# Kernel optimization log

Measured on AMD Instinct MI355X. Metric: run time of the kernel, lower is better.

Reference implementation:

```python
import jax, jax.numpy as jnp
import numpy as np

N_VERTICES = 50000
N_RADIAL = 5
N_ANGULAR = 8
FEATURE_DIM = 64
AMT_TEMPLATES = 64
TEMPLATE_RADIUS = 0.03
ROTATION_DELTA = 1


def create_template_matrix(n_radial, n_angular, radius):
    # Polar grid of template vertices in cartesian coordinates: (R, A, 2)
    radii = radius * (np.arange(1, n_radial + 1) / n_radial)
    angles = 2.0 * np.pi * np.arange(n_angular) / n_angular
    x = radii[:, None] * np.cos(angles)[None, :]
    y = radii[:, None] * np.sin(angles)[None, :]
    return np.stack([x, y], axis=-1).astype(np.float32)


def define_interpolation_coefficients(template_matrix):
    # Gaussian interpolation prior (concrete instance of the abstract method),
    # normalized over all template vertices. Shape: (R, A, R, A)
    R, A, _ = template_matrix.shape
    flat = template_matrix.reshape(R * A, 2)
    d2 = ((flat[:, None, :] - flat[None, :, :]) ** 2).sum(-1)  # (RA, RA)
    sigma = TEMPLATE_RADIUS / N_RADIAL
    w = np.exp(-d2 / (2.0 * sigma ** 2))
    w = w / w.sum(axis=1, keepdims=True)
    return w.reshape(R, A, R, A).astype(np.float32)


def setup_inputs() -> dict:
    key = jax.random.key(0)
    k1, k2, k3, k4, k5, k6, k7 = jax.random.split(key, 7)
    mesh_signal = jax.random.normal(k1, (N_VERTICES, FEATURE_DIM), dtype=jnp.float32)
    # barycentric coordinates: [..., 0] = vertex index (stored as float),
    # [..., 1] = barycentric weight summing to 1 over the 3 triangle corners
    idx = jax.random.randint(k2, (N_VERTICES, N_RADIAL, N_ANGULAR, 3), 0, N_VERTICES)
    w = jax.random.uniform(k3, (N_VERTICES, N_RADIAL, N_ANGULAR, 3), dtype=jnp.float32)
    w = w / jnp.sum(w, axis=-1, keepdims=True)
    bary_coordinates = jnp.stack([idx.astype(jnp.float32), w], axis=-1)
    neighbor_weights = jax.random.normal(
        k4, (AMT_TEMPLATES, N_RADIAL, N_ANGULAR, FEATURE_DIM), dtype=jnp.float32) * 0.05
    center_weights = jax.random.normal(
        k5, (AMT_TEMPLATES, 1, FEATURE_DIM), dtype=jnp.float32) * 0.05
    bias = jax.random.normal(k6, (AMT_TEMPLATES,), dtype=jnp.float32) * 0.05
    tmpl = create_template_matrix(N_RADIAL, N_ANGULAR, TEMPLATE_RADIUS)
    interp_coeff = jnp.asarray(
        define_interpolation_coefficients(tmpl).reshape(N_RADIAL, N_ANGULAR, N_RADIAL * N_ANGULAR))
    return {
        "mesh_signal": mesh_signal,
        "bary_coordinates": bary_coordinates,
        "neighbor_weights": neighbor_weights,
        "center_weights": center_weights,
        "bias": bias,
        "interp_coeff": interp_coeff,
    }


def reference(mesh_signal, bary_coordinates, neighbor_weights, center_weights, bias, interp_coeff):
    N, R, A, _, _ = bary_coordinates.shape
    C = mesh_signal.shape[-1]
    T = neighbor_weights.shape[0]

    # ---- patch operator: barycentric gather + interpolation ----
    idx = bary_coordinates[..., 0].astype(jnp.int32)          # (N, R, A, 3)
    bw = bary_coordinates[..., 1]                              # (N, R, A, 3)
    gathered = mesh_signal[idx]                                # (N, R, A, 3, C)
    interp = jnp.sum(bw[..., None] * gathered, axis=-2)        # (N, R, A, C)

    # ---- prior: matvec with interpolation coefficients ----
    # original: (N,1,1,C,RA) matvec (R,A,RA) -> (N,R,A,C)
    ms = interp.reshape(N, R * A, C)                           # (N, RA, C)
    interp = jnp.einsum('nmc,ram->nrac', ms, interp_coeff)     # (N, R, A, C)

    # ---- center fold: einsum('si,tji->sjt') ----
    conv_center = jnp.einsum('nc,tjc->njt', mesh_signal, center_weights)  # (N, 1, T)

    # ---- neighbor fold over rotations ----
    # roll(interp, shift=r, axis=angular) . W == interp . roll(W, shift=-r, axis=angular)
    rotations = np.arange(0, A, ROTATION_DELTA)
    w_rot = jnp.stack([jnp.roll(neighbor_weights, -int(r), axis=2) for r in rotations])  # (O, T, R, A, C)
    conv_neighbor = jnp.einsum('nrac,otrac->not', interp, w_rot) + bias                  # (N, O, T)

    return jax.nn.relu(conv_center + conv_neighbor)
```

## Files before the change

kernel.cpp:

```cpp
#include <hip/hip_runtime.h>
#include <hip/hip_bf16.h>

#define N_V   50000
#define KTOT  2624
#define NOUT  512
#define NKB   41
#define BM    128
#define BN    256

typedef short v8s __attribute__((ext_vector_type(8)));
typedef float v4f __attribute__((ext_vector_type(4)));
typedef unsigned int v4u __attribute__((ext_vector_type(4)));
typedef unsigned short u16;
typedef unsigned int u32;

__device__ __forceinline__ u16 f2bf(float f) {
    u32 u = __float_as_uint(f);
    return (u16)((u + 0x7FFFu + ((u >> 16) & 1u)) >> 16);
}

__device__ __forceinline__ void gl2lds(const u16* g, u16* l) {
    __builtin_amdgcn_global_load_lds(
        (const __attribute__((address_space(1))) u32*)(uintptr_t)g,
        (__attribute__((address_space(3))) u32*)(uintptr_t)l, 16, 0, 0);
}

__device__ __forceinline__ u32 ipair(u32 pa, u32 pb, u32 pc, float w0, float w1, float w2) {
    float a0 = __uint_as_float(pa << 16), a1 = __uint_as_float(pa & 0xffff0000u);
    float b0 = __uint_as_float(pb << 16), b1 = __uint_as_float(pb & 0xffff0000u);
    float c0 = __uint_as_float(pc << 16), c1 = __uint_as_float(pc & 0xffff0000u);
    float r0 = w0 * a0 + w1 * b0 + w2 * c0;
    float r1 = w0 * a1 + w1 * b1 + w2 * c1;
    return __builtin_amdgcn_perm(__float_as_uint(r1) + 0x8000u,
                                 __float_as_uint(r0) + 0x8000u, 0x07060302u);
}

__global__ void cast_ms(const float* __restrict__ ms, u16* __restrict__ msb,
                        u16* __restrict__ Xc) {
    int i = (blockIdx.x * 256 + threadIdx.x) * 4;
    float4 v = *reinterpret_cast<const float4*>(ms + i);
    ushort4 o;
    o.x = f2bf(v.x); o.y = f2bf(v.y); o.z = f2bf(v.z); o.w = f2bf(v.w);
    *reinterpret_cast<ushort4*>(msb + i) = o;
    if (Xc) {
        int n = i >> 6, c = i & 63;
        *reinterpret_cast<ushort4*>(Xc + (size_t)n * KTOT + 2560 + c) = o;
    }
}

__global__ void build_w2(const float* __restrict__ nw, const float* __restrict__ cw,
                         const float* __restrict__ coeff, u16* __restrict__ w2) {
    int l = blockIdx.x * 256 + threadIdx.x;
    if (l >= NOUT * KTOT) return;
    int j = l / KTOT, k = l - j * KTOT;
    int o = j >> 6, t = j & 63;
    u16 v;
    if (k >= 2560) {
        v = f2bf(cw[t * 64 + (k - 2560)]);
    } else {
        int m = k >> 6, c = k & 63;
        float s = 0.f;
        #pragma unroll
        for (int ra = 0; ra < 40; ++ra) {
            int r = ra >> 3, a = ra & 7;
            s += coeff[ra * 40 + m] * nw[((t * 5 + r) * 8 + ((a + o) & 7)) * 64 + c];
        }
        v = f2bf(s);
    }
    w2[l] = v;
}

__global__ void build_x(const float* __restrict__ bary, const u16* __restrict__ msb,
                        u16* __restrict__ X) {
    u32 t = blockIdx.x * 256 + threadIdx.x;
    u32 n = t / 160u;
    u32 rem = t - n * 160u;
    u32 m = rem >> 2, j = rem & 3;
    const float* bb = bary + (size_t)n * 240 + m * 6;
    float2 p0 = *(const float2*)(bb);
    float2 p1 = *(const float2*)(bb + 2);
    float2 p2 = *(const float2*)(bb + 4);
    u32 jb = j * 32u;
    u32 o0 = ((u32)(int)p0.x) * 128u + jb;
    u32 o1 = ((u32)(int)p1.x) * 128u + jb;
    u32 o2 = ((u32)(int)p2.x) * 128u + jb;
    const char* mb = (const char*)msb;
    v4u a0 = *(const v4u*)(mb + o0), b0 = *(const v4u*)(mb + o0 + 16);
    v4u a1 = *(const v4u*)(mb + o1), b1 = *(const v4u*)(mb + o1 + 16);
    v4u a2 = *(const v4u*)(mb + o2), b2 = *(const v4u*)(mb + o2 + 16);
    v4u c0, c1;
    #pragma unroll
    for (int e = 0; e < 4; ++e) {
        c0[e] = ipair(a0[e], a1[e], a2[e], p0.y, p1.y, p2.y);
        c1[e] = ipair(b0[e], b1[e], b2[e], p0.y, p1.y, p2.y);
    }
    char* xp = (char*)X + (size_t)n * (KTOT * 2) + m * 128 + jb;
    *(v4u*)xp = c0;
    *(v4u*)(xp + 16) = c1;
}

__global__ __launch_bounds__(512, 4)
void gemm2(const u16* __restrict__ X, const u16* __restrict__ w2,
           const float* __restrict__ bias, float* __restrict__ out) {
    __shared__ u16 At[BM * 64];
    __shared__ u16 Bt[BN * 64];

    const int tid  = threadIdx.x;
    const int lane = tid & 63, wave = tid >> 6;
    const int l15  = lane & 15, q = lane >> 4;
    const int wm   = wave >> 2, wn = wave & 3;

    const int id = blockIdx.x;
    const int p  = (id & 7) + 8 * (id >> 4);
    const int by = (id >> 3) & 1;
    if (p >= 391) return;
    const int row0 = p * BM, col0 = by * BN;

    u32 aoff[2];
    #pragma unroll
    for (int h = 0; h < 2; ++h) {
        int slot = wave * 128 + h * 64 + lane;
        int arow = slot >> 3, ablk = (slot & 7) ^ (arow & 7);
        int grow = row0 + arow; if (grow > N_V - 1) grow = N_V - 1;
        aoff[h] = (u32)grow * (u32)KTOT + (u32)(ablk * 8);
    }
    u32 boff[4];
    #pragma unroll
    for (int i = 0; i < 4; ++i) {
        int slot = wave * 256 + i * 64 + lane;
        int brow = slot >> 3, bblk = (slot & 7) ^ (brow & 7);
        boff[i] = (u32)(col0 + brow) * (u32)KTOT + (u32)(bblk * 8);
    }

    const int eq = l15 & 7;
    const u32 a_rd0 = (u32)(wm * 64 + l15) * 128 + (u32)((q ^ eq) * 16);
    const u32 b_rd0 = (u32)(wn * 64 + l15) * 128 + (u32)((q ^ eq) * 16);

    v4f acc[4][4];
    #pragma unroll
    for (int mi = 0; mi < 4; ++mi)
        #pragma unroll
        for (int ni = 0; ni < 4; ++ni)
            acc[mi][ni] = (v4f){0.f, 0.f, 0.f, 0.f};

    #pragma unroll 1
    for (int kb = 0; kb < NKB; ++kb) {
        __syncthreads();
        #pragma unroll
        for (int h = 0; h < 2; ++h)
            gl2lds(X + aoff[h] + kb * 64, &At[wave * 1024 + h * 512]);
        #pragma unroll
        for (int i = 0; i < 4; ++i)
            gl2lds(w2 + boff[i] + kb * 64, &Bt[wave * 2048 + i * 512]);
        __syncthreads();

        const char* atp = (const char*)At;
        const char* btp = (const char*)Bt;
        #pragma unroll
        for (int s = 0; s < 2; ++s) {
            u32 ao = a_rd0 ^ (u32)(s * 64), bo = b_rd0 ^ (u32)(s * 64);
            v8s a_f[4], b_f[4];
            #pragma unroll
            for (int mi = 0; mi < 4; ++mi) a_f[mi] = *(const v8s*)(atp + ao + mi * 2048);
            #pragma unroll
            for (int ni = 0; ni < 4; ++ni) b_f[ni] = *(const v8s*)(btp + bo + ni * 2048);
            #pragma unroll
            for (int mi = 0; mi < 4; ++mi)
                #pragma unroll
                for (int ni = 0; ni < 4; ++ni)
                    acc[mi][ni] = __builtin_amdgcn_mfma_f32_16x16x32_bf16(
                        a_f[mi], b_f[ni], acc[mi][ni], 0, 0, 0);
        }
    }

    float bv[4];
    #pragma unroll
    for (int ni = 0; ni < 4; ++ni) bv[ni] = bias[ni * 16 + l15];
    #pragma unroll
    for (int mi = 0; mi < 4; ++mi) {
        int rbase = row0 + wm * 64 + mi * 16 + q * 4;
        #pragma unroll
        for (int ni = 0; ni < 4; ++ni) {
            int cg = col0 + wn * 64 + ni * 16 + l15;
            #pragma unroll
            for (int rg = 0; rg < 4; ++rg) {
                int rr = rbase + rg;
                if (rr < N_V) {
                    float v = acc[mi][ni][rg] + bv[ni];
                    out[(size_t)rr * NOUT + cg] = v > 0.f ? v : 0.f;
                }
            }
        }
    }
}

__global__ __launch_bounds__(512, 2)
void gemm_fused(const float* __restrict__ bary, const u16* __restrict__ msb,
                const u16* __restrict__ w2, const float* __restrict__ bias,
                float* __restrict__ out) {
    __shared__ u16 At[BM * 64];
    __shared__ u16 Bt[2 * BN * 64];

    const int tid  = threadIdx.x;
    const int lane = tid & 63, wave = tid >> 6;
    const int l15  = lane & 15, q = lane >> 4;
    const int wm   = wave >> 2, wn = wave & 3;

    const int id  = blockIdx.x;
    const int bx  = id % 391, by = id / 391;
    const int row0 = bx * BM, col0 = by * BN;

    const int ar  = tid >> 2;
    const u32 acb = (u32)(tid & 3) * 32;
    int an = row0 + ar; if (an > N_V - 1) an = N_V - 1;
    const u32* brow = (const u32*)bary + (size_t)an * 240;
    const u32 an_off = (u32)an * 128 + acb;

    const int e_a = ar & 7;
    const u32 at_w0 = (u32)ar * 128 + (u32)(((2 * (tid & 3)) ^ e_a) * 16);
    const u32 at_w1 = at_w0 ^ 16;

    const int eq = l15 & 7;
    const u32 a_rd0 = (u32)(wm * 64 + l15) * 128 + (u32)((q ^ eq) * 16);
    const u32 b_rd0 = (u32)(wn * 64 + l15) * 128 + (u32)((q ^ eq) * 16);

    const int rl = lane >> 3;
    const int bl = (lane & 7) ^ rl;

    v4f acc[4][4];
    #pragma unroll
    for (int mi = 0; mi < 4; ++mi)
        #pragma unroll
        for (int ni = 0; ni < 4; ++ni)
            acc[mi][ni] = (v4f){0.f, 0.f, 0.f, 0.f};

    v4u G0_0a, G0_0b, G0_1a, G0_1b, G0_2a, G0_2b;
    v4u G1_0a, G1_0b, G1_1a, G1_1b, G1_2a, G1_2b;
    v4u B0lo, B0hi, B1lo, B1hi;
    float w00, w01, w02, w10, w11, w12;
    v4u cv0, cv1;

#define BARY_LOAD(DLO, DHI, kc) do { \
    u32 _d0 = ((u32)((kc) * 6)) & ~3u; \
    DLO = *(const v4u*)(brow + _d0); \
    DHI = *(const v4u*)(brow + _d0 + 4); } while (0)

#define DECODE_ISSUE(PAR, BLO, BHI, Ga0, Gb0, Ga1, Gb1, Ga2, Gb2, W0, W1, W2) do { \
    u32 uf0, uw0, uf1, uw1, uf2, uw2; \
    if (PAR) { uf0 = BLO[2]; uw0 = BLO[3]; uf1 = BHI[0]; uw1 = BHI[1]; uf2 = BHI[2]; uw2 = BHI[3]; } \
    else     { uf0 = BLO[0]; uw0 = BLO[1]; uf1 = BLO[2]; uw1 = BLO[3]; uf2 = BHI[0]; uw2 = BHI[1]; } \
    u32 _o0 = ((u32)(int)__uint_as_float(uf0) << 7) + acb; \
    u32 _o1 = ((u32)(int)__uint_as_float(uf1) << 7) + acb; \
    u32 _o2 = ((u32)(int)__uint_as_float(uf2) << 7) + acb; \
    const char* _mb = (const char*)msb; \
    Ga0 = *(const v4u*)(_mb + _o0); Gb0 = *(const v4u*)(_mb + _o0 + 16); \
    Ga1 = *(const v4u*)(_mb + _o1); Gb1 = *(const v4u*)(_mb + _o1 + 16); \
    Ga2 = *(const v4u*)(_mb + _o2); Gb2 = *(const v4u*)(_mb + _o2 + 16); \
    W0 = __uint_as_float(uw0); W1 = __uint_as_float(uw1); W2 = __uint_as_float(uw2); } while (0)

#define CONVERT(Ga0, Gb0, Ga1, Gb1, Ga2, Gb2, W0, W1, W2) do { \
    _Pragma("unroll") \
    for (int _j = 0; _j < 4; ++_j) { \
        cv0[_j] = ipair(Ga0[_j], Ga1[_j], Ga2[_j], W0, W1, W2); \
        cv1[_j] = ipair(Gb0[_j], Gb1[_j], Gb2[_j], W0, W1, W2); } } while (0)

#define BLDS(KB_LD, BUF) do { \
    _Pragma("unroll") \
    for (int _ii = 0; _ii < 4; ++_ii) { \
        int _we = wave * 4 + _ii; \
        u32 _src = (u32)(col0 + _we * 8 + rl) * KTOT + (u32)(KB_LD) * 64 + (u32)(bl * 8); \
        gl2lds(w2 + _src, &Bt[(BUF) * (BN * 64) + _we * 512]); } } while (0)

#define AT_STORE() do { \
    *(v4u*)((char*)At + at_w0) = cv0; \
    *(v4u*)((char*)At + at_w1) = cv1; } while (0)

#define MFMA_STEP(BUF) do { \
    const char* _atp = (const char*)At; \
    const char* _btp = (const char*)Bt + (BUF) * (BN * 64 * 2); \
    _Pragma("unroll") \
    for (int _s = 0; _s < 2; ++_s) { \
        u32 _ao = a_rd0 ^ (u32)(_s * 64), _bo = b_rd0 ^ (u32)(_s * 64); \
        v8s _af[4], _bf[4]; \
        _Pragma("unroll") \
        for (int _mi = 0; _mi < 4; ++_mi) _af[_mi] = *(const v8s*)(_atp + _ao + _mi * 2048); \
        _Pragma("unroll") \
        for (int _ni = 0; _ni < 4; ++_ni) _bf[_ni] = *(const v8s*)(_btp + _bo + _ni * 2048); \
        _Pragma("unroll") \
        for (int _mi = 0; _mi < 4; ++_mi) \
            _Pragma("unroll") \
            for (int _ni = 0; _ni < 4; ++_ni) \
                acc[_mi][_ni] = __builtin_amdgcn_mfma_f32_16x16x32_bf16( \
                    _af[_mi], _bf[_ni], acc[_mi][_ni], 0, 0, 0); } } while (0)

#define BAR2_12() asm volatile("s_waitcnt vmcnt(12) lgkmcnt(0)\ns_barrier" ::: "memory")
#define BAR2_10() asm volatile("s_waitcnt vmcnt(10) lgkmcnt(0)\ns_barrier" ::: "memory")
#define BAR2_6()  asm volatile("s_waitcnt vmcnt(6) lgkmcnt(0)\ns_barrier"  ::: "memory")
#define BAR2_4()  asm volatile("s_waitcnt vmcnt(4) lgkmcnt(0)\ns_barrier"  ::: "memory")
#define BAR2_0()  asm volatile("s_waitcnt vmcnt(0) lgkmcnt(0)\ns_barrier"  ::: "memory")
#define BAR1()    asm volatile("s_barrier" ::: "memory")

    BARY_LOAD(B0lo, B0hi, 0);
    DECODE_ISSUE(0, B0lo, B0hi, G0_0a, G0_0b, G0_1a, G0_1b, G0_2a, G0_2b, w00, w01, w02);
    BARY_LOAD(B1lo, B1hi, 1);
    DECODE_ISSUE(1, B1lo, B1hi, G1_0a, G1_0b, G1_1a, G1_1b, G1_2a, G1_2b, w10, w11, w12);
    BARY_LOAD(B0lo, B0hi, 2);
    BLDS(0, 0);

    #pragma unroll 1
    for (int i = 0; i < 20; ++i) {
        {
            const int kb = 2 * i;
            CONVERT(G0_0a, G0_0b, G0_1a, G0_1b, G0_2a, G0_2b, w00, w01, w02);
            if (kb <= 36) BARY_LOAD(B1lo, B1hi, kb + 3);
            if (kb <= 37) {
                DECODE_ISSUE(0, B0lo, B0hi, G0_0a, G0_0b, G0_1a, G0_1b, G0_2a, G0_2b,
                             w00, w01, w02);
            } else if (kb == 38) {
                G0_0a = *(const v4u*)((const char*)msb + an_off);
                G0_0b = *(const v4u*)((const char*)msb + an_off + 16);
            }
            BAR1();
            BLDS(kb + 1, 1);
            AT_STORE();
            if (kb <= 36) BAR2_12(); else BAR2_6();
            MFMA_STEP(0);
        }
        {
            const int kb = 2 * i + 1;
            CONVERT(G1_0a, G1_0b, G1_1a, G1_1b, G1_2a, G1_2b, w10, w11, w12);
            if (kb <= 36) BARY_LOAD(B0lo, B0hi, kb + 3);
            if (kb <= 37)
                DECODE_ISSUE(1, B1lo, B1hi, G1_0a, G1_0b, G1_1a, G1_1b, G1_2a, G1_2b,
                             w10, w11, w12);
            BAR1();
            BLDS(kb + 1, 0);
            AT_STORE();
            if (kb <= 36) BAR2_12();
            else if (kb == 37) BAR2_10();
            else BAR2_4();
            MFMA_STEP(1);
        }
    }
    {
        cv0 = G0_0a; cv1 = G0_0b;
        BAR1();
        AT_STORE();
        BAR2_0();
        MFMA_STEP(0);
    }

    float bv[4];
    #pragma unroll
    for (int ni = 0; ni < 4; ++ni) bv[ni] = bias[ni * 16 + l15];
    #pragma unroll
    for (int mi = 0; mi < 4; ++mi) {
        int rbase = row0 + wm * 64 + mi * 16 + q * 4;
        #pragma unroll
        for (int ni = 0; ni < 4; ++ni) {
            int cg = col0 + wn * 64 + ni * 16 + l15;
            #pragma unroll
            for (int rg = 0; rg < 4; ++rg) {
                int rr = rbase + rg;
                if (rr < N_V) {
                    float v = acc[mi][ni][rg] + bv[ni];
                    out[(size_t)rr * NOUT + cg] = v > 0.f ? v : 0.f;
                }
            }
        }
    }
}

extern "C" void kernel_launch(void* const* d_in, const int* in_sizes, int n_in,
                              void* d_out, int out_size, void* d_ws, size_t ws_size,
                              hipStream_t stream) {
    const float* ms    = (const float*)d_in[0];
    const float* bary  = (const float*)d_in[1];
    const float* nw    = (const float*)d_in[2];
    const float* cw    = (const float*)d_in[3];
    const float* bias  = (const float*)d_in[4];
    const float* coeff = (const float*)d_in[5];
    float* out = (float*)d_out;

    u16* msb = (u16*)d_ws;
    u16* w2  = (u16*)((char*)d_ws + 6400000);
    const size_t x_off  = 9087104;
    const size_t x_need = x_off + (size_t)N_V * KTOT * 2;
    u16* X = (u16*)((char*)d_ws + x_off);

    if (ws_size >= x_need) {
        cast_ms<<<3125, 256, 0, stream>>>(ms, msb, X);
        build_w2<<<(NOUT * KTOT + 255) / 256, 256, 0, stream>>>(nw, cw, coeff, w2);
        build_x<<<31250, 256, 0, stream>>>(bary, msb, X);
        gemm2<<<784, 512, 0, stream>>>(X, w2, bias, out);
    } else {
        cast_ms<<<3125, 256, 0, stream>>>(ms, msb, (u16*)nullptr);
        build_w2<<<(NOUT * KTOT + 255) / 256, 256, 0, stream>>>(nw, cw, coeff, w2);
        gemm_fused<<<782, 512, 0, stream>>>(bary, msb, w2, bias, out);
    }
}
```

Before: 452.7 us.

## Add 256x256-tile GEMM with 4-stage LDS pipeline using dynamic shared memory

Adds a new GEMM kernel that uses 256x256 output tiles with a K-step of 32 and a four-buffer global-to-LDS prefetch ring in 128KB of dynamic shared memory. Compute overlaps with loads three stages ahead, gated by vmcnt waits, and MFMA issue runs under raised wave priority. The larger tile doubles operand reuse per block and halves the grid, at the cost of lower occupancy (two blocks per CU by launch bound, fewer waves in practice because of LDS use) and more accumulator registers. The old GEMM is kept as a fallback if the dynamic LDS attribute cannot be set.

```diff
diff --git a/kernel.cpp b/kernel.cpp
--- a/kernel.cpp
+++ b/kernel.cpp
@@ -7,6 +7,7 @@
 #define NKB   41
 #define BM    128
 #define BN    256
+#define KT32  82
 
 typedef short v8s __attribute__((ext_vector_type(8)));
 typedef float v4f __attribute__((ext_vector_type(4)));
@@ -99,6 +100,108 @@
     *(v4u*)(xp + 16) = c1;
 }
 
+#define WBAR(N) asm volatile("s_waitcnt vmcnt(" #N ")\n\ts_barrier" ::: "memory")
+
+__global__ __launch_bounds__(512, 2)
+void gemm3(const u16* __restrict__ X, const u16* __restrict__ w2,
+           const float* __restrict__ bias, float* __restrict__ out) {
+    extern __shared__ char lds[];
+
+    const int tid  = threadIdx.x;
+    const int lane = tid & 63, wave = tid >> 6;
+    const int l15  = lane & 15, q = lane >> 4;
+    const int wm   = wave >> 2, wn = wave & 3;
+
+    const int id = blockIdx.x;
+    const int p  = (id & 7) + 8 * (id >> 4);
+    const int by = (id >> 3) & 1;
+    if (p >= 196) return;
+    const int row0 = p * 256, col0 = by * 256;
+
+    u32 aoff[2], boff[2];
+    #pragma unroll
+    for (int h = 0; h < 2; ++h) {
+        int slot = (wave * 2 + h) * 64 + lane;
+        int row  = slot >> 2, b = slot & 3;
+        int g    = b ^ ((row >> 1) & 3);
+        int grow = row0 + row; if (grow > N_V - 1) grow = N_V - 1;
+        aoff[h] = (u32)grow * (u32)KTOT + (u32)(g * 8);
+        boff[h] = (u32)(col0 + row) * (u32)KTOT + (u32)(g * 8);
+    }
+
+    const int sw = (l15 >> 1) & 3;
+    const u32 a_rd0 = (u32)(wm * 128 + l15) * 64u + (u32)((q ^ sw) * 16);
+    const u32 b_rd0 = (u32)(wn * 64  + l15) * 64u + (u32)((q ^ sw) * 16);
+
+    v4f acc[8][4];
+    #pragma unroll
+    for (int mi = 0; mi < 8; ++mi)
+        #pragma unroll
+        for (int ni = 0; ni < 4; ++ni)
+            acc[mi][ni] = (v4f){0.f, 0.f, 0.f, 0.f};
+
+#define STG(T, BUF) do { \
+    const u32 _ko = (u32)(T) * 32u; \
+    _Pragma("unroll") \
+    for (int _h = 0; _h < 2; ++_h) { \
+        gl2lds(X  + aoff[_h] + _ko, (u16*)(lds + (BUF) * 16384 + (wave * 2 + _h) * 1024)); \
+        gl2lds(w2 + boff[_h] + _ko, (u16*)(lds + 65536 + (BUF) * 16384 + (wave * 2 + _h) * 1024)); \
+    } } while (0)
+
+#define CMP(BUF) do { \
+    const char* _ap = lds + (BUF) * 16384; \
+    const char* _bp = lds + 65536 + (BUF) * 16384; \
+    v8s _bf[4], _af[8]; \
+    _Pragma("unroll") \
+    for (int _ni = 0; _ni < 4; ++_ni) _bf[_ni] = *(const v8s*)(_bp + b_rd0 + _ni * 1024); \
+    _Pragma("unroll") \
+    for (int _mi = 0; _mi < 8; ++_mi) _af[_mi] = *(const v8s*)(_ap + a_rd0 + _mi * 1024); \
+    __builtin_amdgcn_s_setprio(1); \
+    _Pragma("unroll") \
+    for (int _mi = 0; _mi < 8; ++_mi) \
+        _Pragma("unroll") \
+        for (int _ni = 0; _ni < 4; ++_ni) \
+            acc[_mi][_ni] = __builtin_amdgcn_mfma_f32_16x16x32_bf16( \
+                _af[_mi], _bf[_ni], acc[_mi][_ni], 0, 0, 0); \
+    __builtin_amdgcn_s_setprio(0); \
+} while (0)
+
+    STG(0, 0); STG(1, 1); STG(2, 2);
+
+    #pragma unroll 1
+    for (int t = 0; t < KT32 - 3; ++t) {
+        WBAR(8);
+        STG(t + 3, (t + 3) & 3);
+        CMP(t & 3);
+    }
+    WBAR(8); CMP(3);
+    WBAR(4); CMP(0);
+    WBAR(0); CMP(1);
+
+#undef STG
+#undef CMP
+
+    float bv[4];
+    #pragma unroll
+    for (int ni = 0; ni < 4; ++ni) bv[ni] = bias[ni * 16 + l15];
+    #pragma unroll
+    for (int mi = 0; mi < 8; ++mi) {
+        int rbase = row0 + wm * 128 + mi * 16 + q * 4;
+        #pragma unroll
+        for (int ni = 0; ni < 4; ++ni) {
+            int cg = col0 + wn * 64 + ni * 16 + l15;
+            #pragma unroll
+            for (int rg = 0; rg < 4; ++rg) {
+                int rr = rbase + rg;
+                if (rr < N_V) {
+                    float v = acc[mi][ni][rg] + bv[ni];
+                    out[(size_t)rr * NOUT + cg] = v > 0.f ? v : 0.f;
+                }
+            }
+        }
+    }
+}
+
 __global__ __launch_bounds__(512, 4)
 void gemm2(const u16* __restrict__ X, const u16* __restrict__ w2,
            const float* __restrict__ bias, float* __restrict__ out) {
@@ -389,10 +492,19 @@
     u16* X = (u16*)((char*)d_ws + x_off);
 
     if (ws_size >= x_need) {
+        static int dyn_ok = -1;
+        if (dyn_ok < 0) {
+            dyn_ok = (hipFuncSetAttribute((const void*)gemm3,
+                          hipFuncAttributeMaxDynamicSharedMemorySize,
+                          131072) == hipSuccess) ? 1 : 0;
+        }
         cast_ms<<<3125, 256, 0, stream>>>(ms, msb, X);
         build_w2<<<(NOUT * KTOT + 255) / 256, 256, 0, stream>>>(nw, cw, coeff, w2);
         build_x<<<31250, 256, 0, stream>>>(bary, msb, X);
-        gemm2<<<784, 512, 0, stream>>>(X, w2, bias, out);
+        if (dyn_ok)
+            gemm3<<<400, 512, 131072, stream>>>(X, w2, bias, out);
+        else
+            gemm2<<<784, 512, 0, stream>>>(X, w2, bias, out);
     } else {
         cast_ms<<<3125, 256, 0, stream>>>(ms, msb, (u16*)nullptr);
         build_w2<<<(NOUT * KTOT + 255) / 256, 256, 0, stream>>>(nw, cw, coeff, w2);
```

Result: slower. 464.9 us (+2.7%).

## Replace GEMM with 256x256-tile double-buffered 4-wave MFMA kernel

Applied to the files above, without the earlier changes.

Replaces the 128x256-tile, 8-wave GEMM with a 256x256 tile computed by 4 waves, each holding a 128x128 accumulator block. K is stepped in chunks of 32, and LDS is double-buffered so the global-to-LDS loads for the next step overlap the MFMAs of the current one. The kernel also uses a different XOR swizzle and raises wave priority around the MFMA bursts. The goal is more data reuse per LDS load and better latency hiding, at the cost of heavy register pressure (likely one block per CU) and a coarse grid of 392 active blocks that may balance poorly across CUs.

```diff
diff --git a/kernel.cpp b/kernel.cpp
--- a/kernel.cpp
+++ b/kernel.cpp
@@ -7,6 +7,7 @@
 #define NKB   41
 #define BM    128
 #define BN    256
+#define KT32  82
 
 typedef short v8s __attribute__((ext_vector_type(8)));
 typedef float v4f __attribute__((ext_vector_type(4)));
@@ -99,89 +100,94 @@
     *(v4u*)(xp + 16) = c1;
 }
 
-__global__ __launch_bounds__(512, 4)
-void gemm2(const u16* __restrict__ X, const u16* __restrict__ w2,
+__global__ __launch_bounds__(256, 2)
+void gemm4(const u16* __restrict__ X, const u16* __restrict__ w2,
            const float* __restrict__ bias, float* __restrict__ out) {
-    __shared__ u16 At[BM * 64];
-    __shared__ u16 Bt[BN * 64];
+    __shared__ u16 sh[32768];
 
     const int tid  = threadIdx.x;
     const int lane = tid & 63, wave = tid >> 6;
     const int l15  = lane & 15, q = lane >> 4;
-    const int wm   = wave >> 2, wn = wave & 3;
+    const int wm   = wave >> 1, wn = wave & 1;
 
     const int id = blockIdx.x;
     const int p  = (id & 7) + 8 * (id >> 4);
     const int by = (id >> 3) & 1;
-    if (p >= 391) return;
-    const int row0 = p * BM, col0 = by * BN;
-
-    u32 aoff[2];
-    #pragma unroll
-    for (int h = 0; h < 2; ++h) {
-        int slot = wave * 128 + h * 64 + lane;
-        int arow = slot >> 3, ablk = (slot & 7) ^ (arow & 7);
-        int grow = row0 + arow; if (grow > N_V - 1) grow = N_V - 1;
-        aoff[h] = (u32)grow * (u32)KTOT + (u32)(ablk * 8);
-    }
-    u32 boff[4];
+    if (p >= 196) return;
+    const int row0 = p * 256, col0 = by * 256;
+
+    u32 aoff[4], boff[4];
     #pragma unroll
     for (int i = 0; i < 4; ++i) {
-        int slot = wave * 256 + i * 64 + lane;
-        int brow = slot >> 3, bblk = (slot & 7) ^ (brow & 7);
-        boff[i] = (u32)(col0 + brow) * (u32)KTOT + (u32)(bblk * 8);
-    }
-
-    const int eq = l15 & 7;
-    const u32 a_rd0 = (u32)(wm * 64 + l15) * 128 + (u32)((q ^ eq) * 16);
-    const u32 b_rd0 = (u32)(wn * 64 + l15) * 128 + (u32)((q ^ eq) * 16);
-
-    v4f acc[4][4];
-    #pragma unroll
-    for (int mi = 0; mi < 4; ++mi)
+        int s   = i * 256 + tid;
+        int row = s >> 2, b = s & 3;
+        int g   = b ^ ((row >> 1) & 3);
+        int grow = row0 + row; if (grow > N_V - 1) grow = N_V - 1;
+        aoff[i] = (u32)grow * (u32)KTOT + (u32)(g * 8);
+        boff[i] = (u32)(col0 + row) * (u32)KTOT + (u32)(g * 8);
+    }
+
+    const int sw = (l15 >> 1) & 3;
+    const u32 a_rd0 = (u32)(wm * 128 + l15) * 64u + (u32)((q ^ sw) * 16);
+    const u32 b_rd0 = (u32)(wn * 128 + l15) * 64u + (u32)((q ^ sw) * 16);
+
+    v4f acc[8][8];
+    #pragma unroll
+    for (int mi = 0; mi < 8; ++mi)
         #pragma unroll
-        for (int ni = 0; ni < 4; ++ni)
+        for (int ni = 0; ni < 8; ++ni)
             acc[mi][ni] = (v4f){0.f, 0.f, 0.f, 0.f};
 
+#define STG4(T, BUF) do { \
+    const u32 _ko = (u32)(T) * 32u; \
+    _Pragma("unroll") \
+    for (int _i = 0; _i < 4; ++_i) { \
+        gl2lds(X  + aoff[_i] + _ko, \
+               (u16*)((char*)sh + (BUF) * 16384 + _i * 4096 + wave * 1024)); \
+        gl2lds(w2 + boff[_i] + _ko, \
+               (u16*)((char*)sh + 32768 + (BUF) * 16384 + _i * 4096 + wave * 1024)); \
+    } } while (0)
+
+#define CMP4(BUF) do { \
+    const char* _ap = (const char*)sh + (BUF) * 16384; \
+    const char* _bp = (const char*)sh + 32768 + (BUF) * 16384; \
+    v8s _af[8], _bf[8]; \
+    _Pragma("unroll") \
+    for (int _mi = 0; _mi < 8; ++_mi) _af[_mi] = *(const v8s*)(_ap + a_rd0 + _mi * 1024); \
+    _Pragma("unroll") \
+    for (int _ni = 0; _ni < 8; ++_ni) _bf[_ni] = *(const v8s*)(_bp + b_rd0 + _ni * 1024); \
+    __builtin_amdgcn_s_setprio(1); \
+    _Pragma("unroll") \
+    for (int _mi = 0; _mi < 8; ++_mi) \
+        _Pragma("unroll") \
+        for (int _ni = 0; _ni < 8; ++_ni) \
+            acc[_mi][_ni] = __builtin_amdgcn_mfma_f32_16x16x32_bf16( \
+                _af[_mi], _bf[_ni], acc[_mi][_ni], 0, 0, 0); \
+    __builtin_amdgcn_s_setprio(0); \
+} while (0)
+
+    STG4(0, 0);
     #pragma unroll 1
-    for (int kb = 0; kb < NKB; ++kb) {
-        __syncthreads();
+    for (int t = 0; t < KT32 - 1; ++t) {
+        asm volatile("s_waitcnt vmcnt(0)\n\ts_barrier" ::: "memory");
+        STG4(t + 1, (t + 1) & 1);
+        CMP4(t & 1);
+    }
+    asm volatile("s_waitcnt vmcnt(0)\n\ts_barrier" ::: "memory");
+    CMP4((KT32 - 1) & 1);
+
+#undef STG4
+#undef CMP4
+
+    float bv[8];
+    #pragma unroll
+    for (int ni = 0; ni < 8; ++ni) bv[ni] = bias[(ni & 3) * 16 + l15];
+    #pragma unroll
+    for (int mi = 0; mi < 8; ++mi) {
+        int rbase = row0 + wm * 128 + mi * 16 + q * 4;
         #pragma unroll
-        for (int h = 0; h < 2; ++h)
-            gl2lds(X + aoff[h] + kb * 64, &At[wave * 1024 + h * 512]);
-        #pragma unroll
-        for (int i = 0; i < 4; ++i)
-            gl2lds(w2 + boff[i] + kb * 64, &Bt[wave * 2048 + i * 512]);
-        __syncthreads();
-
-        const char* atp = (const char*)At;
-        const char* btp = (const char*)Bt;
-        #pragma unroll
-        for (int s = 0; s < 2; ++s) {
-            u32 ao = a_rd0 ^ (u32)(s * 64), bo = b_rd0 ^ (u32)(s * 64);
-            v8s a_f[4], b_f[4];
-            #pragma unroll
-            for (int mi = 0; mi < 4; ++mi) a_f[mi] = *(const v8s*)(atp + ao + mi * 2048);
-            #pragma unroll
-            for (int ni = 0; ni < 4; ++ni) b_f[ni] = *(const v8s*)(btp + bo + ni * 2048);
-            #pragma unroll
-            for (int mi = 0; mi < 4; ++mi)
-                #pragma unroll
-                for (int ni = 0; ni < 4; ++ni)
-                    acc[mi][ni] = __builtin_amdgcn_mfma_f32_16x16x32_bf16(
-                        a_f[mi], b_f[ni], acc[mi][ni], 0, 0, 0);
-        }
-    }
-
-    float bv[4];
-    #pragma unroll
-    for (int ni = 0; ni < 4; ++ni) bv[ni] = bias[ni * 16 + l15];
-    #pragma unroll
-    for (int mi = 0; mi < 4; ++mi) {
-        int rbase = row0 + wm * 64 + mi * 16 + q * 4;
-        #pragma unroll
-        for (int ni = 0; ni < 4; ++ni) {
-            int cg = col0 + wn * 64 + ni * 16 + l15;
+        for (int ni = 0; ni < 8; ++ni) {
+            int cg = col0 + wn * 128 + ni * 16 + l15;
             #pragma unroll
             for (int rg = 0; rg < 4; ++rg) {
                 int rr = rbase + rg;
@@ -392,7 +398,7 @@
         cast_ms<<<3125, 256, 0, stream>>>(ms, msb, X);
         build_w2<<<(NOUT * KTOT + 255) / 256, 256, 0, stream>>>(nw, cw, coeff, w2);
         build_x<<<31250, 256, 0, stream>>>(bary, msb, X);
-        gemm2<<<784, 512, 0, stream>>>(X, w2, bias, out);
+        gemm4<<<400, 256, 0, stream>>>(X, w2, bias, out);
     } else {
         cast_ms<<<3125, 256, 0, stream>>>(ms, msb, (u16*)nullptr);
         build_w2<<<(NOUT * KTOT + 255) / 256, 256, 0, stream>>>(nw, cw, coeff, w2);
```

After: 1.458 ms. 3.22x slower.

## Merge weight build and gather-interpolate into one launch with wave-per-sample gather

Applied to the files above, without the earlier changes.

Combines the build_w2 and build_x kernels into a single launch in which the first block range builds the folded weight matrix and the rest build the interpolated X. The X gather now assigns one wave per (vertex, template-point) sample, with each lane reading one bf16 channel, in a grid-stride loop over persistent waves. This replaces per-thread 32-byte vector gathers with 2-byte per-lane loads. The goal is to remove one launch and let the two independent preprocessing jobs overlap, at the risk of narrower memory transactions and more loop overhead.

```diff
diff --git a/kernel.cpp b/kernel.cpp
--- a/kernel.cpp
+++ b/kernel.cpp
@@ -7,6 +7,8 @@
 #define NKB   41
 #define BM    128
 #define BN    256
+#define NW2BLK 5248
+#define NXBLK  8192
 
 typedef short v8s __attribute__((ext_vector_type(8)));
 typedef float v4f __attribute__((ext_vector_type(4)));
@@ -17,6 +19,10 @@
 __device__ __forceinline__ u16 f2bf(float f) {
     u32 u = __float_as_uint(f);
     return (u16)((u + 0x7FFFu + ((u >> 16) & 1u)) >> 16);
+}
+
+__device__ __forceinline__ float bf2f(u16 v) {
+    return __uint_as_float((u32)v << 16);
 }
 
 __device__ __forceinline__ void gl2lds(const u16* g, u16* l) {
@@ -48,55 +54,56 @@
     }
 }
 
-__global__ void build_w2(const float* __restrict__ nw, const float* __restrict__ cw,
-                         const float* __restrict__ coeff, u16* __restrict__ w2) {
-    int l = blockIdx.x * 256 + threadIdx.x;
-    if (l >= NOUT * KTOT) return;
-    int j = l / KTOT, k = l - j * KTOT;
-    int o = j >> 6, t = j & 63;
-    u16 v;
-    if (k >= 2560) {
-        v = f2bf(cw[t * 64 + (k - 2560)]);
-    } else {
-        int m = k >> 6, c = k & 63;
-        float s = 0.f;
-        #pragma unroll
-        for (int ra = 0; ra < 40; ++ra) {
-            int r = ra >> 3, a = ra & 7;
-            s += coeff[ra * 40 + m] * nw[((t * 5 + r) * 8 + ((a + o) & 7)) * 64 + c];
-        }
-        v = f2bf(s);
-    }
-    w2[l] = v;
-}
-
-__global__ void build_x(const float* __restrict__ bary, const u16* __restrict__ msb,
-                        u16* __restrict__ X) {
-    u32 t = blockIdx.x * 256 + threadIdx.x;
-    u32 n = t / 160u;
-    u32 rem = t - n * 160u;
-    u32 m = rem >> 2, j = rem & 3;
-    const float* bb = bary + (size_t)n * 240 + m * 6;
-    float2 p0 = *(const float2*)(bb);
-    float2 p1 = *(const float2*)(bb + 2);
-    float2 p2 = *(const float2*)(bb + 4);
-    u32 jb = j * 32u;
-    u32 o0 = ((u32)(int)p0.x) * 128u + jb;
-    u32 o1 = ((u32)(int)p1.x) * 128u + jb;
-    u32 o2 = ((u32)(int)p2.x) * 128u + jb;
-    const char* mb = (const char*)msb;
-    v4u a0 = *(const v4u*)(mb + o0), b0 = *(const v4u*)(mb + o0 + 16);
-    v4u a1 = *(const v4u*)(mb + o1), b1 = *(const v4u*)(mb + o1 + 16);
-    v4u a2 = *(const v4u*)(mb + o2), b2 = *(const v4u*)(mb + o2 + 16);
-    v4u c0, c1;
-    #pragma unroll
-    for (int e = 0; e < 4; ++e) {
-        c0[e] = ipair(a0[e], a1[e], a2[e], p0.y, p1.y, p2.y);
-        c1[e] = ipair(b0[e], b1[e], b2[e], p0.y, p1.y, p2.y);
-    }
-    char* xp = (char*)X + (size_t)n * (KTOT * 2) + m * 128 + jb;
-    *(v4u*)xp = c0;
-    *(v4u*)(xp + 16) = c1;
+__global__ __launch_bounds__(256)
+void build_xw(const float* __restrict__ nw, const float* __restrict__ cw,
+              const float* __restrict__ coeff, u16* __restrict__ w2,
+              const float* __restrict__ bary, const u16* __restrict__ msb,
+              u16* __restrict__ X) {
+    const int bid = blockIdx.x;
+    if (bid < NW2BLK) {
+        int l = bid * 256 + threadIdx.x;
+        if (l >= NOUT * KTOT) return;
+        int j = l / KTOT, k = l - j * KTOT;
+        int o = j >> 6, t = j & 63;
+        u16 v;
+        if (k >= 2560) {
+            v = f2bf(cw[t * 64 + (k - 2560)]);
+        } else {
+            int m = k >> 6, c = k & 63;
+            float s = 0.f;
+            #pragma unroll
+            for (int ra = 0; ra < 40; ++ra) {
+                int r = ra >> 3, a = ra & 7;
+                s += coeff[ra * 40 + m] * nw[((t * 5 + r) * 8 + ((a + o) & 7)) * 64 + c];
+            }
+            v = f2bf(s);
+        }
+        w2[l] = v;
+        return;
+    }
+
+    const int xb   = bid - NW2BLK;
+    const int lane = threadIdx.x & 63;
+    const u32 wv   = (u32)__builtin_amdgcn_readfirstlane(threadIdx.x >> 6);
+    const u32 wid  = (u32)xb * 4u + wv;
+    const u32 NWAVES = (u32)NXBLK * 4u;
+
+    #pragma unroll 2
+    for (u32 u = wid; u < 2000000u; u += NWAVES) {
+        const float* bb = bary + (size_t)u * 6;
+        float i0 = bb[0], w0 = bb[1];
+        float i1 = bb[2], w1 = bb[3];
+        float i2 = bb[4], w2f = bb[5];
+        u32 o0 = (u32)(int)i0 * 64u + (u32)lane;
+        u32 o1 = (u32)(int)i1 * 64u + (u32)lane;
+        u32 o2 = (u32)(int)i2 * 64u + (u32)lane;
+        float a = bf2f(msb[o0]);
+        float b = bf2f(msb[o1]);
+        float c = bf2f(msb[o2]);
+        float r = w0 * a + w1 * b + w2f * c;
+        u32 n = u / 40u, m = u - n * 40u;
+        X[(size_t)n * KTOT + m * 64u + (u32)lane] = f2bf(r);
+    }
 }
 
 __global__ __launch_bounds__(512, 4)
@@ -390,12 +397,11 @@
 
     if (ws_size >= x_need) {
         cast_ms<<<3125, 256, 0, stream>>>(ms, msb, X);
-        build_w2<<<(NOUT * KTOT + 255) / 256, 256, 0, stream>>>(nw, cw, coeff, w2);
-        build_x<<<31250, 256, 0, stream>>>(bary, msb, X);
+        build_xw<<<NW2BLK + NXBLK, 256, 0, stream>>>(nw, cw, coeff, w2, bary, msb, X);
         gemm2<<<784, 512, 0, stream>>>(X, w2, bias, out);
     } else {
         cast_ms<<<3125, 256, 0, stream>>>(ms, msb, (u16*)nullptr);
-        build_w2<<<(NOUT * KTOT + 255) / 256, 256, 0, stream>>>(nw, cw, coeff, w2);
+        build_xw<<<NW2BLK, 256, 0, stream>>>(nw, cw, coeff, w2, bary, msb, (u16*)nullptr);
         gemm_fused<<<782, 512, 0, stream>>>(bary, msb, w2, bias, out);
     }
 }
```

Result: slower. 618.2 us (+36.6%).
